# Optimization experiments

Hardware: AMD Instinct MI355X
Metric: run time of the kernel (lower is better)

The kernel has to match this reference:

```python
import jax, jax.numpy as jnp
import numpy as np


def setup_inputs() -> dict:
    key = jax.random.key(0)
    ks = jax.random.split(key, 6)
    N, D_IN, H, DH, N_ITEM = 4096, 512, 8, 128, 256
    x = jax.random.normal(ks[0], (N, D_IN), dtype=jnp.float32)
    y = jax.random.normal(ks[1], (N, D_IN), dtype=jnp.float32)
    # linear1/linear2 have NonNeg kernel constraint -> nonnegative weights
    W1 = jax.random.uniform(ks[2], (D_IN, H * DH), dtype=jnp.float32) * 0.05
    W2 = jax.random.uniform(ks[3], (D_IN, H * DH), dtype=jnp.float32) * 0.05
    W3 = jax.random.normal(ks[4], (D_IN, H * DH), dtype=jnp.float32) * 0.05
    # 1x1 conv with 1 output filter over the head axis == weighted sum over heads
    conv_w = jax.random.normal(ks[5], (H,), dtype=jnp.float32)
    return {"x": x, "y": y, "W1": W1, "W2": W2, "W3": W3,
            "conv_w": conv_w, "nItem": N_ITEM}


def reference(x, y, W1, W2, W3, conv_w, nItem):
    N = x.shape[0]
    H = conv_w.shape[0]
    Dh = W1.shape[1] // H
    nSet = N // nItem
    inv_sqrt = 1.0 / jnp.sqrt(jnp.asarray(Dh, dtype=x.dtype))

    q = (x @ W1).reshape(N, H, Dh).transpose(1, 0, 2)   # [H, N, Dh]
    k = (y @ W2).reshape(N, H, Dh).transpose(1, 0, 2)   # [H, N, Dh]
    v = (y @ W3).reshape(N, H, Dh).transpose(1, 0, 2)   # [H, N, Dh]

    # Full cross-set scores, as in the original: [H, N, N]
    scores = jnp.einsum('hnd,hmd->hnm', q, k) * inv_sqrt

    # Block-diagonal y2 matmul == per-set segmented matmul:
    # newx[h, n, s*Dh:(s+1)*Dh] = scores[h, n, s*nItem:(s+1)*nItem] @ v_set_s
    scores_s = scores.reshape(H, N, nSet, nItem)
    v_s = v.reshape(H, nSet, nItem, Dh)
    newx = jnp.einsum('hnsi,hsid->hnsd', scores_s, v_s) / nItem  # [H, N, nSet, Dh]

    # 1x1 conv mixing heads (single output filter, no bias)
    mixed = jnp.einsum('hnsd,h->nsd', newx, conv_w)  # [N, nSet, Dh]

    # isOnlySelf=False branch: reshape [N, nSet*Dh] -> [N, nSet, Dh]
    return mixed
```

## Files before the change

### kernel.cpp

```cpp
#include <hip/hip_runtime.h>
#include <stdint.h>
#include <stddef.h>


typedef short short8 __attribute__((ext_vector_type(8)));
typedef float f32x4 __attribute__((ext_vector_type(4)));

#define AS1 __attribute__((address_space(1)))
#define AS3 __attribute__((address_space(3)))

__device__ __forceinline__ void gl_lds16(const void* g, void* l) {
    __builtin_amdgcn_global_load_lds((AS1 void*)(uintptr_t)g, (AS3 void*)l, 16, 0, 0);
}

__device__ __forceinline__ short f2bf(float f) {
    union { float f; unsigned u; } v; v.f = f;
    unsigned r = v.u + 0x7FFFu + ((v.u >> 16) & 1u);
    return (short)(r >> 16);
}

__global__ __launch_bounds__(256)
void prep(const float* __restrict__ x, const float* __restrict__ y,
          const float* __restrict__ W1, const float* __restrict__ W2,
          const float* __restrict__ W3, short* __restrict__ xb,
          short* __restrict__ yb, short* __restrict__ w1t,
          short* __restrict__ w23t) {
    const int b = blockIdx.x, tid = threadIdx.x;
    if (b < 2048) {
        const float* in = (b < 1024) ? x : y;
        short* o = (b < 1024) ? xb : yb;
        const int i = (b & 1023) * 256 + tid;
        const float4* p = (const float4*)in + (size_t)i * 2;
        float4 a = p[0], c4 = p[1];
        short8 s8;
        s8[0] = f2bf(a.x);  s8[1] = f2bf(a.y);
        s8[2] = f2bf(a.z);  s8[3] = f2bf(a.w);
        s8[4] = f2bf(c4.x); s8[5] = f2bf(c4.y);
        s8[6] = f2bf(c4.z); s8[7] = f2bf(c4.w);
        *((short8*)o + i) = s8;
        return;
    }
    __shared__ float t[32][33];
    const float* W; short* Wt; int b3;
    if (b < 3072) {
        const int b2 = b - 2048;
        const int z = b2 >> 9;
        W = z ? W3 : W2;
        Wt = w23t + (size_t)z * 1024 * 512;
        b3 = b2 & 511;
    } else {
        W = W1; Wt = w1t; b3 = b - 3072;
    }
    const int bx = (b3 & 31) * 32, by = (b3 >> 5) * 32;
    const int tx = tid & 31, ty = tid >> 5;
    #pragma unroll
    for (int j = 0; j < 4; ++j)
        t[ty + j * 8][tx] = W[(size_t)(by + ty + j * 8) * 1024 + bx + tx];
    __syncthreads();
    #pragma unroll
    for (int j = 0; j < 4; ++j)
        Wt[(size_t)(bx + ty + j * 8) * 512 + by + tx] = f2bf(t[tx][ty + j * 8]);
}

template <int OUTMODE>
__device__ __forceinline__
void gemm_tile(const short* __restrict__ A, int lda,
               const short* __restrict__ Bt, int ldb,
               void* __restrict__ Cout, int ldc, int K,
               int bx, int by, float scale, char* smem) {
    short* sA = (short*)smem;
    short* sB = (short*)(smem + 8192);

    const int tid = threadIdx.x;
    const int wave = tid >> 6, lane = tid & 63;
    const int quad = lane >> 4, ml = lane & 15;
    const int m0 = by * 128, n0 = bx * 128;
    const int wm0 = (wave >> 1) * 64, wn0 = (wave & 1) * 64;
    const int srow = lane >> 2, skoff = (lane & 3) * 8;

    f32x4 acc[4][4];
    #pragma unroll
    for (int i = 0; i < 4; ++i)
        #pragma unroll
        for (int j = 0; j < 4; ++j) {
            acc[i][j][0] = 0.f; acc[i][j][1] = 0.f;
            acc[i][j][2] = 0.f; acc[i][j][3] = 0.f;
        }

    for (int kt = 0; kt < K; kt += 32) {
        #pragma unroll
        for (int ci = 0; ci < 4; ++ci) {
            const int c = wave + ci * 4;
            if (c < 8)
                gl_lds16(A + (size_t)(m0 + c * 16 + srow) * lda + kt + skoff,
                         (char*)sA + c * 1024 + lane * 16);
            else
                gl_lds16(Bt + (size_t)(n0 + (c - 8) * 16 + srow) * ldb + kt + skoff,
                         (char*)sB + (c - 8) * 1024 + lane * 16);
        }
        __syncthreads();

        short8 af[4], bfr[4];
        #pragma unroll
        for (int mt = 0; mt < 4; ++mt)
            af[mt] = *(const short8*)(sA + (wm0 + mt * 16 + ml) * 32 + quad * 8);
        #pragma unroll
        for (int nt = 0; nt < 4; ++nt)
            bfr[nt] = *(const short8*)(sB + (wn0 + nt * 16 + ml) * 32 + quad * 8);

        #pragma unroll
        for (int mt = 0; mt < 4; ++mt)
            #pragma unroll
            for (int nt = 0; nt < 4; ++nt)
                acc[mt][nt] = __builtin_amdgcn_mfma_f32_16x16x32_bf16(
                    af[mt], bfr[nt], acc[mt][nt], 0, 0, 0);
        __syncthreads();
    }

    #pragma unroll
    for (int mt = 0; mt < 4; ++mt)
        #pragma unroll
        for (int nt = 0; nt < 4; ++nt) {
            const int col = n0 + wn0 + nt * 16 + ml;
            #pragma unroll
            for (int r = 0; r < 4; ++r) {
                const int row = m0 + wm0 + mt * 16 + quad * 4 + r;
                float v = acc[mt][nt][r];
                if (OUTMODE == 2) v *= scale;
                if (OUTMODE == 0)
                    ((float*)Cout)[(size_t)row * ldc + col] = v;
                else
                    ((short*)Cout)[(size_t)row * ldc + col] = f2bf(v);
            }
        }
}

__global__ __launch_bounds__(256)
void stage_b(const short* __restrict__ yb, const short* __restrict__ w23t,
             const short* __restrict__ xb, const short* __restrict__ w1t,
             short* __restrict__ kvt, short* __restrict__ qb) {
    __shared__ char smem[16384];
    const int b = blockIdx.x;
    if (b < 512) {
        gemm_tile<1>(w23t, 512, yb, 512, kvt, 4096, 512,
                     b & 31, b >> 5, 1.f, smem);
    } else {
        const int b2 = b - 512;
        gemm_tile<1>(xb, 512, w1t, 512, qb, 1024, 512,
                     b2 & 7, b2 >> 3, 1.f, smem);
    }
}

__global__ __launch_bounds__(256)
void build_u(const short* __restrict__ kvt, const float* __restrict__ cw,
             short* __restrict__ Ut) {
    __shared__ char smem[16384];
    const int s = blockIdx.x, h = blockIdx.y;
    const float scale = cw[h] * (0.08838834764831845f / 256.0f);
    gemm_tile<2>(kvt + (size_t)(1024 + h * 128) * 4096 + s * 256, 4096,
                 kvt + (size_t)(h * 128) * 4096 + s * 256, 4096,
                 Ut + (size_t)(s * 128) * 1024 + h * 128, 1024, 256,
                 0, 0, scale, smem);
}

__global__ __launch_bounds__(256)
void gemm_out(const short* __restrict__ qb, const short* __restrict__ Ut,
              float* __restrict__ out) {
    __shared__ char smem[16384];
    gemm_tile<0>(qb, 1024, Ut, 1024, out, 2048, 1024,
                 blockIdx.x, blockIdx.y, 1.f, smem);
}

extern "C" void kernel_launch(void* const* d_in, const int* in_sizes, int n_in,
                              void* d_out, int out_size, void* d_ws, size_t ws_size,
                              hipStream_t stream) {
    const float* x  = (const float*)d_in[0];
    const float* y  = (const float*)d_in[1];
    const float* W1 = (const float*)d_in[2];
    const float* W2 = (const float*)d_in[3];
    const float* W3 = (const float*)d_in[4];
    const float* cw = (const float*)d_in[5];
    float* out = (float*)d_out;

    short* xb   = (short*)d_ws;
    short* yb   = xb   + (size_t)4096 * 512;
    short* w1t  = yb   + (size_t)4096 * 512;
    short* w23t = w1t  + (size_t)1024 * 512;
    short* kvt  = w23t + (size_t)2048 * 512;
    short* qb   = kvt  + (size_t)2048 * 4096;
    short* Ut   = qb   + (size_t)4096 * 1024;

    prep<<<3584, 256, 0, stream>>>(x, y, W1, W2, W3, xb, yb, w1t, w23t);
    stage_b<<<768, 256, 0, stream>>>(yb, w23t, xb, w1t, kvt, qb);
    build_u<<<dim3(16, 8), 256, 0, stream>>>(kvt, cw, Ut);
    gemm_out<<<dim3(16, 32), 256, 0, stream>>>(qb, Ut, out);
}
```

Baseline: 141.6 us.

## Fuse projection, U-build and output GEMMs into one flag-synchronized persistent kernel

Merges the stage_b, build_u and gemm_out launches into a single kernel whose block ranges run each stage. Dependencies between stages are enforced with per-tile global atomic flags, set with release stores and polled with acquire loads plus sleep. The aim is to cut kernel launch gaps and tail idle time, so later stages can start once their own inputs are ready. In exchange it adds a memset, spin-wait overhead, and a deadlock risk if waiting blocks are scheduled before their producers. The launch bounds also change to request three blocks per SM.

Result: slower. 550.5 us (+288.7%).

```diff
diff --git a/kernel.cpp b/kernel.cpp
--- a/kernel.cpp
+++ b/kernel.cpp
@@ -18,6 +18,12 @@
     unsigned r = v.u + 0x7FFFu + ((v.u >> 16) & 1u);
     return (short)(r >> 16);
 }
+
+__device__ __forceinline__ void wait_ge(const int* p, int want) {
+    while (__hip_atomic_load(p, __ATOMIC_ACQUIRE, __HIP_MEMORY_SCOPE_AGENT) < want)
+        __builtin_amdgcn_s_sleep(8);
+}
+
 
 __global__ __launch_bounds__(256)
 void prep(const float* __restrict__ x, const float* __restrict__ y,
@@ -135,40 +141,56 @@
         }
 }
 
-__global__ __launch_bounds__(256)
-void stage_b(const short* __restrict__ yb, const short* __restrict__ w23t,
-             const short* __restrict__ xb, const short* __restrict__ w1t,
-             short* __restrict__ kvt, short* __restrict__ qb) {
+__global__ __launch_bounds__(256, 3)
+void mega(const short* __restrict__ xb, const short* __restrict__ yb,
+          const short* __restrict__ w1t, const short* __restrict__ w23t,
+          const float* __restrict__ cw, short* __restrict__ kvt,
+          short* __restrict__ qb, short* __restrict__ Ut,
+          float* __restrict__ out, int* __restrict__ flags) {
     __shared__ char smem[16384];
-    const int b = blockIdx.x;
+    const int b = blockIdx.x, tid = threadIdx.x;
+
     if (b < 512) {
-        gemm_tile<1>(w23t, 512, yb, 512, kvt, 4096, 512,
-                     b & 31, b >> 5, 1.f, smem);
+        const int by = b >> 5, bx = b & 31;
+        gemm_tile<1>(w23t, 512, yb, 512, kvt, 4096, 512, bx, by, 1.f, smem);
+        __threadfence();
+        __syncthreads();
+        if (tid == 0)
+            __hip_atomic_store(&flags[(by << 5) | bx], 1,
+                               __ATOMIC_RELEASE, __HIP_MEMORY_SCOPE_AGENT);
+    } else if (b < 768) {
+        const int b2 = b - 512;
+        const int my = b2 >> 3, nx = b2 & 7;
+        gemm_tile<1>(xb, 512, w1t, 512, qb, 1024, 512, nx, my, 1.f, smem);
+        __threadfence();
+        __syncthreads();
+        if (tid == 0)
+            __hip_atomic_fetch_add(&flags[512 + my], 1,
+                                   __ATOMIC_RELEASE, __HIP_MEMORY_SCOPE_AGENT);
+    } else if (b < 896) {
+        const int b2 = b - 768;
+        const int s = b2 & 15, h = b2 >> 4;
+        wait_ge(&flags[(h << 5) | (2 * s)], 1);
+        wait_ge(&flags[(h << 5) | (2 * s + 1)], 1);
+        wait_ge(&flags[((8 + h) << 5) | (2 * s)], 1);
+        wait_ge(&flags[((8 + h) << 5) | (2 * s + 1)], 1);
+        const float scale = cw[h] * (0.08838834764831845f / 256.0f);
+        gemm_tile<2>(kvt + (size_t)(1024 + h * 128) * 4096 + s * 256, 4096,
+                     kvt + (size_t)(h * 128) * 4096 + s * 256, 4096,
+                     Ut + (size_t)(s * 128) * 1024 + h * 128, 1024, 256,
+                     0, 0, scale, smem);
+        __threadfence();
+        __syncthreads();
+        if (tid == 0)
+            __hip_atomic_fetch_add(&flags[544 + s], 1,
+                                   __ATOMIC_RELEASE, __HIP_MEMORY_SCOPE_AGENT);
     } else {
-        const int b2 = b - 512;
-        gemm_tile<1>(xb, 512, w1t, 512, qb, 1024, 512,
-                     b2 & 7, b2 >> 3, 1.f, smem);
-    }
-}
-
-__global__ __launch_bounds__(256)
-void build_u(const short* __restrict__ kvt, const float* __restrict__ cw,
-             short* __restrict__ Ut) {
-    __shared__ char smem[16384];
-    const int s = blockIdx.x, h = blockIdx.y;
-    const float scale = cw[h] * (0.08838834764831845f / 256.0f);
-    gemm_tile<2>(kvt + (size_t)(1024 + h * 128) * 4096 + s * 256, 4096,
-                 kvt + (size_t)(h * 128) * 4096 + s * 256, 4096,
-                 Ut + (size_t)(s * 128) * 1024 + h * 128, 1024, 256,
-                 0, 0, scale, smem);
-}
-
-__global__ __launch_bounds__(256)
-void gemm_out(const short* __restrict__ qb, const short* __restrict__ Ut,
-              float* __restrict__ out) {
-    __shared__ char smem[16384];
-    gemm_tile<0>(qb, 1024, Ut, 1024, out, 2048, 1024,
-                 blockIdx.x, blockIdx.y, 1.f, smem);
+        const int b2 = b - 896;
+        const int s = b2 & 15, my = b2 >> 4;
+        wait_ge(&flags[512 + my], 8);
+        wait_ge(&flags[544 + s], 8);
+        gemm_tile<0>(qb, 1024, Ut, 1024, out, 2048, 1024, s, my, 1.f, smem);
+    }
 }
 
 extern "C" void kernel_launch(void* const* d_in, const int* in_sizes, int n_in,
@@ -182,16 +204,17 @@
     const float* cw = (const float*)d_in[5];
     float* out = (float*)d_out;
 
-    short* xb   = (short*)d_ws;
-    short* yb   = xb   + (size_t)4096 * 512;
-    short* w1t  = yb   + (size_t)4096 * 512;
-    short* w23t = w1t  + (size_t)1024 * 512;
-    short* kvt  = w23t + (size_t)2048 * 512;
-    short* qb   = kvt  + (size_t)2048 * 4096;
-    short* Ut   = qb   + (size_t)4096 * 1024;
-
+    char* ws = (char*)d_ws;
+    short* xb   = (short*)(ws);
+    short* yb   = (short*)(ws + (4u << 20));
+    short* w1t  = (short*)(ws + (8u << 20));
+    short* w23t = (short*)(ws + (9u << 20));
+    short* kvt  = (short*)(ws + (11u << 20));
+    short* qb   = (short*)(ws + (27u << 20));
+    short* Ut   = (short*)(ws + (35u << 20));
+    int*  flags = (int*)(ws + (48u << 20));
+
+    hipMemsetAsync(flags, 0, 560 * sizeof(int), stream);
     prep<<<3584, 256, 0, stream>>>(x, y, W1, W2, W3, xb, yb, w1t, w23t);
-    stage_b<<<768, 256, 0, stream>>>(yb, w23t, xb, w1t, kvt, qb);
-    build_u<<<dim3(16, 8), 256, 0, stream>>>(kvt, cw, Ut);
-    gemm_out<<<dim3(16, 32), 256, 0, stream>>>(qb, Ut, out);
-}
+    mega<<<1408, 256, 0, stream>>>(xb, yb, w1t, w23t, cw, kvt, qb, Ut, out, flags);
+}
```
